# Kernel optimization log

Hardware: AMD Instinct MI355X
Metric: run time of the kernel (lower is better)

The kernel has to match this reference:

```python
import jax, jax.numpy as jnp
import numpy as np

ALPHA = 0.99   # config.alpha_grape
GAMMA = 0.999  # config.gamma
LAMBD = 0.7    # config.lambd_grape
T, A = 262144, 64


def setup_inputs() -> dict:
    key = jax.random.key(0)
    ks = jax.random.split(key, 7)
    q = jax.random.normal(ks[0], (T + 1, A), jnp.float32)
    q_tar = jax.random.normal(ks[1], (T + 1, A), jnp.float32)
    # pi / mu are probability distributions over actions (softmax of logits)
    pi = jax.nn.softmax(jax.random.normal(ks[2], (T + 1, A), jnp.float32), axis=-1)
    mu_t = jax.nn.softmax(jax.random.normal(ks[3], (T, A), jnp.float32), axis=-1)
    a_t = jax.random.randint(ks[4], (T,), 0, A, dtype=jnp.int32)
    r_t = jax.random.normal(ks[5], (T,), jnp.float32)
    done_t = jax.random.randint(ks[6], (T,), 0, 2, dtype=jnp.int32)
    return dict(q=q, q_tar=q_tar, pi=pi, a_t=a_t, r_t=r_t, mu_t=mu_t, done_t=done_t)


def reference(q, q_tar, pi, a_t, r_t, mu_t, done_t):
    # GRAPE.compute_targets
    l = q.shape[0] - 1
    idx = jnp.arange(l)
    pi_t, pi_tp1 = pi[:-1], pi[1:]
    q_t, q_tp1 = q[:-1], q_tar[1:]
    q_t_a = q_t[idx, a_t]                              # [T]
    v_t = jnp.sum(pi_t * q_t, axis=1)                  # [T]
    v_tp1 = jnp.sum(pi_tp1 * q_tp1, axis=1)            # [T]
    done_f = done_t.astype(q.dtype)
    q_t_a_est = r_t + (1.0 - done_f) * GAMMA * v_tp1
    td_error = q_t_a_est - q_t_a
    rho_t_a = pi_t[idx, a_t] / mu_t[idx, a_t]
    c_t_a = LAMBD * jnp.clip(rho_t_a, 0.0, 1.0)

    # backward-in-time first-order recurrence over y'
    def step(y_prime, xs):
        est, td, rho, c, d = xs
        y = jnp.where(d > 0.5, 0.0, y_prime)           # reset at episode end
        g = est + y
        y_new = LAMBD * GAMMA * rho * td + GAMMA * c * y
        return y_new, g

    _, g_q = jax.lax.scan(
        step, jnp.float32(0.0),
        (q_t_a_est, td_error, rho_t_a, c_t_a, done_f),
        reverse=True,
    )
    targets_q = g_q + ALPHA * (q_t_a - v_t)            # [T]
    advantages = (1.0 - ALPHA) * (q_t - v_t[:, None])  # [T, A]
    return targets_q, advantages
```

## Files before the change

kernel.cpp:

```cpp
#include <hip/hip_runtime.h>

#define GAMMA 0.999f
#define LAMBD 0.7f
#define ALPHA 0.99f

constexpr int A_DIM = 64;
constexpr int CH    = 128;

__device__ __forceinline__ float pick4(const float4& v, int k) {
    float lo = (k & 1) ? v.y : v.x;
    float hi = (k & 1) ? v.w : v.z;
    return (k & 2) ? hi : lo;
}

__global__ void k_row(const float* __restrict__ q,
                      const float* __restrict__ q_tar,
                      const float* __restrict__ pi,
                      const int*   __restrict__ a_t,
                      const float* __restrict__ r_t,
                      const float* __restrict__ mu_t,
                      const int*   __restrict__ done_t,
                      float*  __restrict__ adv_out,
                      float4* __restrict__ scr,
                      int T)
{
    int wave = (blockIdx.x * blockDim.x + threadIdx.x) >> 6;
    int lane = threadIdx.x & 63;
    int sub  = lane >> 4;
    int li   = lane & 15;
    int r    = wave * 4 + sub;
    if (r >= T) return;

    int base = r * A_DIM + li * 4;

    float4 pi4  = *(const float4*)&pi[base];
    float4 q4   = *(const float4*)&q[base];
    float4 pip4 = *(const float4*)&pi[base + A_DIM];
    float4 qp4  = *(const float4*)&q_tar[base + A_DIM];
    float4 mu4  = *(const float4*)&mu_t[base];

    float s0 = pi4.x*q4.x  + pi4.y*q4.y  + pi4.z*q4.z  + pi4.w*q4.w;
    float s1 = pip4.x*qp4.x + pip4.y*qp4.y + pip4.z*qp4.z + pip4.w*qp4.w;
    #pragma unroll
    for (int off = 1; off < 16; off <<= 1) {
        s0 += __shfl_xor(s0, off);
        s1 += __shfl_xor(s1, off);
    }

    int   a  = a_t[r];
    float rr = r_t[r];
    float dn = (float)done_t[r];

    int src = (sub << 4) | (a >> 2);
    int ac  = a & 3;
    float q_t_a  = __shfl(pick4(q4,  ac), src);
    float pi_t_a = __shfl(pick4(pi4, ac), src);
    float mu_a   = __shfl(pick4(mu4, ac), src);

    float kmask = 1.0f - dn;
    float est = rr + kmask * (GAMMA * s1);
    float td  = est - q_t_a;
    float rho = pi_t_a / mu_a;
    float c   = LAMBD * fminf(fmaxf(rho, 0.0f), 1.0f);

    float Acoef = (LAMBD * GAMMA) * rho * td;
    float Bp    = kmask * (GAMMA * c);
    float E     = est + ALPHA * (q_t_a - s0);

    float4 adv4;
    adv4.x = (1.0f - ALPHA) * (q4.x - s0);
    adv4.y = (1.0f - ALPHA) * (q4.y - s0);
    adv4.z = (1.0f - ALPHA) * (q4.z - s0);
    adv4.w = (1.0f - ALPHA) * (q4.w - s0);
    *(float4*)&adv_out[base] = adv4;

    if (li == 0) scr[r] = make_float4(E, kmask, Acoef, Bp);
}

__global__ void k_suffix(const float4* __restrict__ scr,
                         float2* __restrict__ sufx,
                         float2* __restrict__ cab, int T)
{
    int wave = (blockIdx.x * blockDim.x + threadIdx.x) >> 6;
    int lane = threadIdx.x & 63;
    int nch  = T / CH;
    if (wave >= nch) return;
    int base = wave * CH + lane * 2;

    float4 e0 = scr[base];
    float4 e1 = scr[base + 1];

    float Ai = e0.z + e0.w * e1.z;
    float Bi = e0.w * e1.w;

    #pragma unroll
    for (int off = 1; off < 64; off <<= 1) {
        float An = __shfl_down(Ai, off);
        float Bn = __shfl_down(Bi, off);
        if (lane + off < 64) {
            Ai = Ai + Bi * An;
            Bi = Bi * Bn;
        }
    }
    float Xa = __shfl_down(Ai, 1);
    float Xb = __shfl_down(Bi, 1);
    if (lane == 63) { Xa = 0.0f; Xb = 1.0f; }

    sufx[base + 1] = make_float2(Xa, Xb);
    sufx[base]     = make_float2(e1.z + e1.w * Xa, e1.w * Xb);

    if (lane == 0) cab[wave] = make_float2(Ai, Bi);
}

__global__ void k_scan(const float2* __restrict__ cab,
                       float* __restrict__ ybound, int nch)
{
    __shared__ float sA[1024], sB[1024];
    int i = threadIdx.x;
    float2 p0 = cab[2 * i];
    float2 p1 = cab[2 * i + 1];
    float Ai = p0.x + p0.y * p1.x;
    float Bi = p0.y * p1.y;
    sA[i] = Ai; sB[i] = Bi;
    __syncthreads();
    for (int off = 1; off < 1024; off <<= 1) {
        float An = 0.0f, Bn = 1.0f;
        if (i + off < 1024) { An = sA[i + off]; Bn = sB[i + off]; }
        __syncthreads();
        Ai = Ai + Bi * An;
        Bi = Bi * Bn;
        sA[i] = Ai; sB[i] = Bi;
        __syncthreads();
    }
    ybound[2 * i] = Ai;
    float yNext = (i + 1 < 1024) ? sA[i + 1] : 0.0f;
    ybound[2 * i + 1] = p1.x + p1.y * yNext;
    if (i == 0) ybound[nch] = 0.0f;
}

__global__ void k_final(const float4* __restrict__ scr,
                        const float2* __restrict__ sufx,
                        const float* __restrict__ ybound,
                        float* __restrict__ targets, int T)
{
    int t = blockIdx.x * blockDim.x + threadIdx.x;
    if (t >= T) return;
    float ye = ybound[(t >> 7) + 1];
    float2 sx = sufx[t];
    float4 v  = scr[t];
    float y_tp1 = sx.x + sx.y * ye;
    targets[t] = v.x + v.y * y_tp1;
}

extern "C" void kernel_launch(void* const* d_in, const int* in_sizes, int n_in,
                              void* d_out, int out_size, void* d_ws, size_t ws_size,
                              hipStream_t stream) {
    const float* q     = (const float*)d_in[0];
    const float* q_tar = (const float*)d_in[1];
    const float* pi    = (const float*)d_in[2];
    const int*   a_t   = (const int*)  d_in[3];
    const float* r_t   = (const float*)d_in[4];
    const float* mu_t  = (const float*)d_in[5];
    const int*   done_t= (const int*)  d_in[6];

    const int T   = in_sizes[3];
    const int nch = T / CH;

    float* targets = (float*)d_out;
    float* adv     = (float*)d_out + T;

    char* ws = (char*)d_ws;
    float4* scr    = (float4*)ws;                                  ws += (size_t)16 * T;
    float2* sufxb  = (float2*)ws;                                  ws += (size_t)8  * T;
    float2* cab    = (float2*)ws;                                  ws += (size_t)8  * nch;
    float*  ybound = (float*)ws;

    {
        int blocks = T / 16;
        k_row<<<blocks, 256, 0, stream>>>(q, q_tar, pi, a_t, r_t, mu_t, done_t,
                                          adv, scr, T);
    }
    k_suffix<<<nch / 4, 256, 0, stream>>>(scr, sufxb, cab, T);
    k_scan<<<1, 1024, 0, stream>>>(cab, ybound, nch);
    k_final<<<(T + 255) / 256, 256, 0, stream>>>(scr, sufxb, ybound, targets, T);
}
```

Before: 73.79 us.

## Fuse per-chunk suffix scan into row kernel via shared memory

The row kernel now processes a 128-row chunk per block. It keeps the per-row recurrence coefficients in shared memory and runs the intra-chunk suffix scan there, removing the separate suffix kernel. Only a combined float2 (u,w) per row is written to global memory, so k_final reads 8 bytes per row instead of 24, and the 16-byte scratch array is dropped. Each block also issues two rows' loads before computing, to increase memory-level parallelism. The cost is lower occupancy and a serial single-wave scan phase inside each block.

Result: no change. 73.39 us (-0.5%).

```diff
diff --git a/kernel.cpp b/kernel.cpp
--- a/kernel.cpp
+++ b/kernel.cpp
@@ -13,103 +13,127 @@
     return (k & 2) ? hi : lo;
 }
 
-__global__ void k_row(const float* __restrict__ q,
-                      const float* __restrict__ q_tar,
-                      const float* __restrict__ pi,
-                      const int*   __restrict__ a_t,
-                      const float* __restrict__ r_t,
-                      const float* __restrict__ mu_t,
-                      const int*   __restrict__ done_t,
-                      float*  __restrict__ adv_out,
-                      float4* __restrict__ scr,
-                      int T)
-{
-    int wave = (blockIdx.x * blockDim.x + threadIdx.x) >> 6;
-    int lane = threadIdx.x & 63;
-    int sub  = lane >> 4;
-    int li   = lane & 15;
-    int r    = wave * 4 + sub;
-    if (r >= T) return;
-
+struct RowRegs {
+    float4 pi4, q4, pip4, qp4, mu4;
+    int   a;
+    float rr, dn;
+};
+
+__device__ __forceinline__ void row_load(const float* __restrict__ q,
+                                         const float* __restrict__ q_tar,
+                                         const float* __restrict__ pi,
+                                         const float* __restrict__ mu_t,
+                                         const int* __restrict__ a_t,
+                                         const float* __restrict__ r_t,
+                                         const int* __restrict__ done_t,
+                                         int r, int li, RowRegs& R)
+{
     int base = r * A_DIM + li * 4;
-
-    float4 pi4  = *(const float4*)&pi[base];
-    float4 q4   = *(const float4*)&q[base];
-    float4 pip4 = *(const float4*)&pi[base + A_DIM];
-    float4 qp4  = *(const float4*)&q_tar[base + A_DIM];
-    float4 mu4  = *(const float4*)&mu_t[base];
-
-    float s0 = pi4.x*q4.x  + pi4.y*q4.y  + pi4.z*q4.z  + pi4.w*q4.w;
-    float s1 = pip4.x*qp4.x + pip4.y*qp4.y + pip4.z*qp4.z + pip4.w*qp4.w;
+    R.pi4  = *(const float4*)&pi[base];
+    R.q4   = *(const float4*)&q[base];
+    R.pip4 = *(const float4*)&pi[base + A_DIM];
+    R.qp4  = *(const float4*)&q_tar[base + A_DIM];
+    R.mu4  = *(const float4*)&mu_t[base];
+    R.a  = a_t[r];
+    R.rr = r_t[r];
+    R.dn = (float)done_t[r];
+}
+
+__device__ __forceinline__ void row_compute(const RowRegs& R, int sub, int li, int gbase,
+                                            float* __restrict__ adv_out,
+                                            float4* sEKAB, int lrow)
+{
+    float s0 = R.pi4.x*R.q4.x  + R.pi4.y*R.q4.y  + R.pi4.z*R.q4.z  + R.pi4.w*R.q4.w;
+    float s1 = R.pip4.x*R.qp4.x + R.pip4.y*R.qp4.y + R.pip4.z*R.qp4.z + R.pip4.w*R.qp4.w;
     #pragma unroll
     for (int off = 1; off < 16; off <<= 1) {
         s0 += __shfl_xor(s0, off);
         s1 += __shfl_xor(s1, off);
     }
-
-    int   a  = a_t[r];
-    float rr = r_t[r];
-    float dn = (float)done_t[r];
-
-    int src = (sub << 4) | (a >> 2);
-    int ac  = a & 3;
-    float q_t_a  = __shfl(pick4(q4,  ac), src);
-    float pi_t_a = __shfl(pick4(pi4, ac), src);
-    float mu_a   = __shfl(pick4(mu4, ac), src);
-
-    float kmask = 1.0f - dn;
-    float est = rr + kmask * (GAMMA * s1);
-    float td  = est - q_t_a;
-    float rho = pi_t_a / mu_a;
+    int src = (sub << 4) | (R.a >> 2);
+    int ac  = R.a & 3;
+    float qa = __shfl(pick4(R.q4,  ac), src);
+    float pa = __shfl(pick4(R.pi4, ac), src);
+    float ma = __shfl(pick4(R.mu4, ac), src);
+
+    float kmask = 1.0f - R.dn;
+    float est = R.rr + kmask * (GAMMA * s1);
+    float td  = est - qa;
+    float rho = pa / ma;
     float c   = LAMBD * fminf(fmaxf(rho, 0.0f), 1.0f);
 
-    float Acoef = (LAMBD * GAMMA) * rho * td;
-    float Bp    = kmask * (GAMMA * c);
-    float E     = est + ALPHA * (q_t_a - s0);
-
     float4 adv4;
-    adv4.x = (1.0f - ALPHA) * (q4.x - s0);
-    adv4.y = (1.0f - ALPHA) * (q4.y - s0);
-    adv4.z = (1.0f - ALPHA) * (q4.z - s0);
-    adv4.w = (1.0f - ALPHA) * (q4.w - s0);
-    *(float4*)&adv_out[base] = adv4;
-
-    if (li == 0) scr[r] = make_float4(E, kmask, Acoef, Bp);
-}
-
-__global__ void k_suffix(const float4* __restrict__ scr,
-                         float2* __restrict__ sufx,
-                         float2* __restrict__ cab, int T)
-{
-    int wave = (blockIdx.x * blockDim.x + threadIdx.x) >> 6;
-    int lane = threadIdx.x & 63;
-    int nch  = T / CH;
-    if (wave >= nch) return;
-    int base = wave * CH + lane * 2;
-
-    float4 e0 = scr[base];
-    float4 e1 = scr[base + 1];
-
-    float Ai = e0.z + e0.w * e1.z;
-    float Bi = e0.w * e1.w;
-
-    #pragma unroll
-    for (int off = 1; off < 64; off <<= 1) {
-        float An = __shfl_down(Ai, off);
-        float Bn = __shfl_down(Bi, off);
-        if (lane + off < 64) {
-            Ai = Ai + Bi * An;
-            Bi = Bi * Bn;
+    adv4.x = (1.0f - ALPHA) * (R.q4.x - s0);
+    adv4.y = (1.0f - ALPHA) * (R.q4.y - s0);
+    adv4.z = (1.0f - ALPHA) * (R.q4.z - s0);
+    adv4.w = (1.0f - ALPHA) * (R.q4.w - s0);
+    *(float4*)&adv_out[gbase] = adv4;
+
+    if (li == 0)
+        sEKAB[lrow] = make_float4(est + ALPHA * (qa - s0),
+                                  kmask,
+                                  (LAMBD * GAMMA) * rho * td,
+                                  kmask * (GAMMA * c));
+}
+
+__global__ __launch_bounds__(256, 4)
+void k_row(const float* __restrict__ q,
+           const float* __restrict__ q_tar,
+           const float* __restrict__ pi,
+           const int*   __restrict__ a_t,
+           const float* __restrict__ r_t,
+           const float* __restrict__ mu_t,
+           const int*   __restrict__ done_t,
+           float*  __restrict__ adv_out,
+           float2* __restrict__ comb,
+           float2* __restrict__ cab)
+{
+    __shared__ float4 sEKAB[CH];
+    __shared__ float2 sUW[CH];
+
+    int tid  = threadIdx.x;
+    int wave = tid >> 6;
+    int lane = tid & 63;
+    int sub  = lane >> 4;
+    int li   = lane & 15;
+    int R0   = blockIdx.x * CH;
+
+    #pragma unroll 2
+    for (int i = 0; i < 8; i += 2) {
+        int lrowA = wave * 32 + i * 4 + sub;
+        int lrowB = lrowA + 4;
+        int rA = R0 + lrowA;
+        int rB = R0 + lrowB;
+        RowRegs Ra, Rb;
+        row_load(q, q_tar, pi, mu_t, a_t, r_t, done_t, rA, li, Ra);
+        row_load(q, q_tar, pi, mu_t, a_t, r_t, done_t, rB, li, Rb);
+        row_compute(Ra, sub, li, rA * A_DIM + li * 4, adv_out, sEKAB, lrowA);
+        row_compute(Rb, sub, li, rB * A_DIM + li * 4, adv_out, sEKAB, lrowB);
+    }
+    __syncthreads();
+
+    if (wave == 0) {
+        float4 e0 = sEKAB[2 * lane];
+        float4 e1 = sEKAB[2 * lane + 1];
+        float Ai = e0.z + e0.w * e1.z;
+        float Bi = e0.w * e1.w;
+        #pragma unroll
+        for (int off = 1; off < 64; off <<= 1) {
+            float An = __shfl_down(Ai, off);
+            float Bn = __shfl_down(Bi, off);
+            if (lane + off < 64) { Ai += Bi * An; Bi *= Bn; }
         }
-    }
-    float Xa = __shfl_down(Ai, 1);
-    float Xb = __shfl_down(Bi, 1);
-    if (lane == 63) { Xa = 0.0f; Xb = 1.0f; }
-
-    sufx[base + 1] = make_float2(Xa, Xb);
-    sufx[base]     = make_float2(e1.z + e1.w * Xa, e1.w * Xb);
-
-    if (lane == 0) cab[wave] = make_float2(Ai, Bi);
+        float Xa = __shfl_down(Ai, 1);
+        float Xb = __shfl_down(Bi, 1);
+        if (lane == 63) { Xa = 0.0f; Xb = 1.0f; }
+        sUW[2 * lane + 1] = make_float2(e1.x + e1.y * Xa, e1.y * Xb);
+        float Sa = e1.z + e1.w * Xa;
+        float Sb = e1.w * Xb;
+        sUW[2 * lane]     = make_float2(e0.x + e0.y * Sa, e0.y * Sb);
+        if (lane == 0) cab[blockIdx.x] = make_float2(Ai, Bi);
+    }
+    __syncthreads();
+    if (tid < CH) comb[R0 + tid] = sUW[tid];
 }
 
 __global__ void k_scan(const float2* __restrict__ cab,
@@ -138,18 +162,15 @@
     if (i == 0) ybound[nch] = 0.0f;
 }
 
-__global__ void k_final(const float4* __restrict__ scr,
-                        const float2* __restrict__ sufx,
+__global__ void k_final(const float2* __restrict__ comb,
                         const float* __restrict__ ybound,
                         float* __restrict__ targets, int T)
 {
     int t = blockIdx.x * blockDim.x + threadIdx.x;
     if (t >= T) return;
     float ye = ybound[(t >> 7) + 1];
-    float2 sx = sufx[t];
-    float4 v  = scr[t];
-    float y_tp1 = sx.x + sx.y * ye;
-    targets[t] = v.x + v.y * y_tp1;
+    float2 uw = comb[t];
+    targets[t] = uw.x + uw.y * ye;
 }
 
 extern "C" void kernel_launch(void* const* d_in, const int* in_sizes, int n_in,
@@ -170,17 +191,12 @@
     float* adv     = (float*)d_out + T;
 
     char* ws = (char*)d_ws;
-    float4* scr    = (float4*)ws;                                  ws += (size_t)16 * T;
-    float2* sufxb  = (float2*)ws;                                  ws += (size_t)8  * T;
-    float2* cab    = (float2*)ws;                                  ws += (size_t)8  * nch;
+    float2* comb   = (float2*)ws;            ws += (size_t)8 * T;
+    float2* cab    = (float2*)ws;            ws += (size_t)8 * nch;
     float*  ybound = (float*)ws;
 
-    {
-        int blocks = T / 16;
-        k_row<<<blocks, 256, 0, stream>>>(q, q_tar, pi, a_t, r_t, mu_t, done_t,
-                                          adv, scr, T);
-    }
-    k_suffix<<<nch / 4, 256, 0, stream>>>(scr, sufxb, cab, T);
+    k_row<<<nch, 256, 0, stream>>>(q, q_tar, pi, a_t, r_t, mu_t, done_t,
+                                   adv, comb, cab);
     k_scan<<<1, 1024, 0, stream>>>(cab, ybound, nch);
-    k_final<<<(T + 255) / 256, 256, 0, stream>>>(scr, sufxb, ybound, targets, T);
-}
+    k_final<<<(T + 255) / 256, 256, 0, stream>>>(comb, ybound, targets, T);
+}
```
